# Kernel tuning notes

Measured on AMD Instinct MI355X. Metric: run time of the kernel, lower is better.

The kernel has to match this reference:

```python
import jax, jax.numpy as jnp
import numpy as np

H = 1024        # hidden_size
I = 512         # moe_intermediate_size
E = 16          # n_routed_experts
K = 2           # num_experts_per_tok
N_SHARED = 2    # n_shared_experts
IS = I * N_SHARED  # shared expert intermediate
B, S = 2, 2048


def setup_inputs() -> dict:
    key = jax.random.key(0)
    ks = jax.random.split(key, 9)
    sc = 0.02
    return {
        "hidden_states": jax.random.normal(ks[0], (B, S, H), jnp.float32),
        "router_w":     jax.random.normal(ks[1], (E, H), jnp.float32) * sc,
        "expert_gate":  jax.random.normal(ks[2], (E, H, I), jnp.float32) * sc,
        "expert_up":    jax.random.normal(ks[3], (E, H, I), jnp.float32) * sc,
        "expert_down":  jax.random.normal(ks[4], (E, I, H), jnp.float32) * sc,
        "shared_gate":  jax.random.normal(ks[5], (H, IS), jnp.float32) * sc,
        "shared_up":    jax.random.normal(ks[6], (H, IS), jnp.float32) * sc,
        "shared_down":  jax.random.normal(ks[7], (IS, H), jnp.float32) * sc,
    }


def reference(hidden_states, router_w, expert_gate, expert_up, expert_down,
              shared_gate, shared_up, shared_down):
    orig_shape = hidden_states.shape
    x = hidden_states.reshape(-1, H)            # [T, H]
    T = x.shape[0]

    # --- MoEGate: softmax router scores, top-k, normalized weights ---
    scores = jax.nn.softmax(x @ router_w.T, axis=-1)        # [T, E]
    topk_w, topk_idx = jax.lax.top_k(scores, K)             # [T, K]
    topk_w = topk_w / jnp.sum(topk_w, axis=-1, keepdims=True)  # norm_topk_prob

    # Sparse combine weights as dense [T, E] gate matrix (scatter of top-k).
    gates = jnp.zeros((T, E), x.dtype).at[jnp.arange(T)[:, None], topk_idx].add(topk_w)

    # --- Routed experts: gated SiLU MLP per expert, weighted combine ---
    g = jnp.einsum('th,ehi->tei', x, expert_gate)           # [T, E, I]
    u = jnp.einsum('th,ehi->tei', x, expert_up)             # [T, E, I]
    a = jax.nn.silu(g) * u                                  # [T, E, I]
    y = jnp.einsum('tei,eih,te->th', a, expert_down, gates) # [T, H]

    # --- Shared experts ---
    s = (jax.nn.silu(x @ shared_gate) * (x @ shared_up)) @ shared_down  # [T, H]

    return (y + s).reshape(orig_shape)
```

## Files before the change

### kernel.cpp

```cpp
#include <hip/hip_runtime.h>
#include <hip/hip_bf16.h>
#include <math.h>

#define H_DIM 1024
#define I_DIM 512
#define E_NUM 16
#define T_TOK 4096
#define IS_DIM 1024
#define MAX_GU 1152
#define MAX_DN 1792
#define CSTR 32

typedef unsigned short u16;
typedef __attribute__((ext_vector_type(8))) short short8;
typedef __attribute__((ext_vector_type(4))) float floatx4;

__device__ __forceinline__ float bf2f(u16 u) {
    union { unsigned int u; float f; } c; c.u = ((unsigned int)u) << 16; return c.f;
}
__device__ __forceinline__ u16 f2bf(float f) {
    union { float f; unsigned int u; } c; c.f = f;
    unsigned int r = (c.u + 0x7fffu + ((c.u >> 16) & 1u)) >> 16;
    return (u16)r;
}
__device__ __forceinline__ void gld16(const u16* g, u16* l) {
    __builtin_amdgcn_global_load_lds(
        (const __attribute__((address_space(1))) unsigned int*)g,
        (__attribute__((address_space(3))) unsigned int*)l, 16, 0, 0);
}

__global__ __launch_bounds__(256)
void k_transpose(const float* wg, const float* wu, const float* wd,
                 const float* sg, const float* su, const float* sd,
                 u16* wgt, u16* wut, u16* wdt, u16* sgt, u16* sut, u16* sdt)
{
    int bx = blockIdx.x;
    const float* src; u16* dst; int R, C, local;
    if (bx < 2048)      { src = wg; dst = wgt; R = 1024; C = 512;  local = bx; }
    else if (bx < 4096) { src = wu; dst = wut; R = 1024; C = 512;  local = bx - 2048; }
    else if (bx < 6144) { src = wd; dst = wdt; R = 512;  C = 1024; local = bx - 4096; }
    else if (bx < 6400) { src = sg; dst = sgt; R = 1024; C = 1024; local = bx - 6144; }
    else if (bx < 6656) { src = su; dst = sut; R = 1024; C = 1024; local = bx - 6400; }
    else                { src = sd; dst = sdt; R = 1024; C = 1024; local = bx - 6656; }
    int tpm = (R >> 6) * (C >> 6);
    int mat = local / tpm;
    int tl_ = local - mat * tpm;
    int tcn = C >> 6;
    int tr = tl_ / tcn, tc = tl_ - (tl_ / tcn) * tcn;
    src += (size_t)mat * R * C;
    dst += (size_t)mat * R * C;

    __shared__ u16 tile[64][65];
    int t = threadIdx.x;
    int r0 = t >> 2, c0 = (t & 3) * 16;
    const float* sp = src + (size_t)(tr * 64 + r0) * C + tc * 64 + c0;
    #pragma unroll
    for (int j = 0; j < 16; j += 4) {
        float4 v = *(const float4*)(sp + j);
        tile[r0][c0 + j + 0] = f2bf(v.x);
        tile[r0][c0 + j + 1] = f2bf(v.y);
        tile[r0][c0 + j + 2] = f2bf(v.z);
        tile[r0][c0 + j + 3] = f2bf(v.w);
    }
    __syncthreads();
    int cW = t >> 2, rW = (t & 3) * 16;
    u16 tmp[16];
    #pragma unroll
    for (int j = 0; j < 16; ++j) tmp[j] = tile[rW + j][cW];
    u16* dp = dst + (size_t)(tc * 64 + cW) * R + tr * 64 + rW;
    *(uint4*)(dp)     = *(const uint4*)(tmp);
    *(uint4*)(dp + 8) = *(const uint4*)(tmp + 8);
}

__global__ __launch_bounds__(256)
void k_xconv(const float* x, u16* xb)
{
    int i = blockIdx.x * 256 + threadIdx.x;
    float4 v = ((const float4*)x)[i];
    u16 o[4] = { f2bf(v.x), f2bf(v.y), f2bf(v.z), f2bf(v.w) };
    ((uint2*)xb)[i] = *(const uint2*)o;
}

__global__ __launch_bounds__(256)
void k_router(const float* x, const float* rw, float* topkw, int* elist, int* cnt)
{
    int lane = threadIdx.x & 63;
    int wv = threadIdx.x >> 6;
    int t = blockIdx.x * 4 + wv;
    const float* xr = x + (size_t)t * H_DIM;
    float xv[16];
    #pragma unroll
    for (int j = 0; j < 16; ++j) xv[j] = xr[j * 64 + lane];
    float sc[E_NUM];
    #pragma unroll
    for (int e = 0; e < E_NUM; ++e) sc[e] = 0.f;
    #pragma unroll
    for (int e = 0; e < E_NUM; ++e) {
        const float* rr = rw + e * H_DIM;
        #pragma unroll
        for (int j = 0; j < 16; ++j) sc[e] += xv[j] * rr[j * 64 + lane];
    }
    #pragma unroll
    for (int off = 32; off > 0; off >>= 1) {
        float tmp[E_NUM];
        #pragma unroll
        for (int e = 0; e < E_NUM; ++e) tmp[e] = __shfl_xor(sc[e], off, 64);
        #pragma unroll
        for (int e = 0; e < E_NUM; ++e) sc[e] += tmp[e];
    }
    if (lane == 0) {
        float b1 = -1e30f, b2 = -1e30f; int i1 = 0, i2 = 0;
        #pragma unroll
        for (int e = 0; e < E_NUM; ++e) {
            if (sc[e] > b1) { b2 = b1; i2 = i1; b1 = sc[e]; i1 = e; }
            else if (sc[e] > b2) { b2 = sc[e]; i2 = e; }
        }
        float w1 = 1.f / (1.f + __expf(b2 - b1));
        float w2 = 1.f - w1;
        topkw[t * 2]     = w1;
        topkw[t * 2 + 1] = w2;
        int p1 = atomicAdd(&cnt[i1 * CSTR], 1); elist[i1 * T_TOK + p1] = (t << 1);
        int p2 = atomicAdd(&cnt[i2 * CSTR], 1); elist[i2 * T_TOK + p2] = (t << 1) | 1;
    }
}

__global__ void k_prefix(const int* cnt, int* base,
                         int* gu_desc, int* gu_count, int* dn_desc, int* dn_count)
{
    __shared__ int mts_s[E_NUM], moff_s[E_NUM];
    int lane = threadIdx.x;
    if (lane == 0) {
        int b = 0, mo = 0;
        for (int e = 0; e < E_NUM; ++e) {
            int mts = (cnt[e * CSTR] + 127) >> 7;
            base[e] = b; b += mts << 7;
            mts_s[e] = mts; moff_s[e] = mo; mo += mts;
        }
        *gu_count = 512 + mo * 8;
        *dn_count = 512 + mo * 16;
    }
    __syncthreads();
    for (int i = lane; i < 512; i += 64) {
        int mt = i >> 4, cb = i & 15;
        int d = (1 << 31) | (mt << 8) | cb;
        gu_desc[i] = d;
        dn_desc[i] = d;
    }
    if (lane < E_NUM) {
        int e = lane, mts = mts_s[e], mo = moff_s[e];
        for (int mt = 0; mt < mts; ++mt) {
            #pragma unroll
            for (int cb = 0; cb < 8; ++cb)
                gu_desc[512 + (mo + mt) * 8 + cb] = (e << 16) | (mt << 8) | cb;
            #pragma unroll
            for (int nb = 0; nb < 16; ++nb)
                dn_desc[512 + (mo + mt) * 16 + nb] = (e << 16) | (mt << 8) | nb;
        }
    }
}

__global__ __launch_bounds__(256, 2)
void k_gateup(const u16* xb, const u16* wgt, const u16* wut,
              const u16* sgt, const u16* sut,
              const int* elist, const int* cnt, const int* base,
              const int* gu_desc, const int* gu_count,
              u16* act, u16* sact)
{
    int bi = blockIdx.x;
    if (bi >= *gu_count) return;
    int d = gu_desc[bi];
    int kind = ((unsigned)d) >> 31;
    int e = (d >> 16) & 15, mt = (d >> 8) & 255, cb = d & 255;

    __shared__ u16 lA[128 * 64], lG[64 * 64], lU[64 * 64];
    int tid = threadIdx.x, lane = tid & 63, w = tid >> 6;
    int srow = lane >> 2, scp = lane & 3;

    const u16* gb = kind ? sgt : (wgt + (size_t)e * I_DIM * H_DIM);
    const u16* ub = kind ? sut : (wut + (size_t)e * I_DIM * H_DIM);
    int c = cnt[e * CSTR];

    const u16 *gA[2], *gG, *gU;
    u16 *dA[2], *dG, *dU;
    #pragma unroll
    for (int jj = 0; jj < 2; ++jj) {
        int call = w * 2 + jj;
        int row = call * 16 + srow;
        int gc = scp ^ ((row >> 1) & 3);
        int tok;
        if (kind) tok = mt * 128 + row;
        else {
            int p = mt * 128 + row;
            int pc = p < c ? p : c - 1;
            tok = elist[e * T_TOK + pc] >> 1;
        }
        gA[jj] = xb + (size_t)tok * H_DIM + gc * 8;
        dA[jj] = lA + call * 512;
    }
    {
        int row = w * 16 + srow;
        int gc = scp ^ ((row >> 1) & 3);
        gG = gb + (size_t)(cb * 64 + row) * H_DIM + gc * 8;
        gU = ub + (size_t)(cb * 64 + row) * H_DIM + gc * 8;
        dG = lG + w * 512;
        dU = lU + w * 512;
    }

    int wr = w >> 1, wc = w & 1;
    int quad = lane >> 4, l15 = lane & 15;
    const u16 *fA[4], *fG[2], *fU[2];
    #pragma unroll
    for (int i = 0; i < 4; ++i) {
        int r = wr * 64 + i * 16 + l15;
        fA[i] = lA + r * 32 + (quad ^ ((r >> 1) & 3)) * 8;
    }
    #pragma unroll
    for (int j = 0; j < 2; ++j) {
        int n = wc * 32 + j * 16 + l15;
        fG[j] = lG + n * 32 + (quad ^ ((n >> 1) & 3)) * 8;
        fU[j] = lU + n * 32 + (quad ^ ((n >> 1) & 3)) * 8;
    }

    floatx4 accg[4][2], accu[4][2];
    #pragma unroll
    for (int i = 0; i < 4; ++i)
        #pragma unroll
        for (int j = 0; j < 2; ++j)
            #pragma unroll
            for (int r = 0; r < 4; ++r) { accg[i][j][r] = 0.f; accu[i][j][r] = 0.f; }

    for (int s = 0; s < H_DIM / 64; ++s) {
        #pragma unroll
        for (int q = 0; q < 2; ++q) {
            gld16(gA[0] + q * 32, dA[0] + q * 4096);
            gld16(gA[1] + q * 32, dA[1] + q * 4096);
            gld16(gG + q * 32, dG + q * 2048);
            gld16(gU + q * 32, dU + q * 2048);
        }
        gA[0] += 64; gA[1] += 64; gG += 64; gU += 64;
        __syncthreads();
        #pragma unroll
        for (int q = 0; q < 2; ++q) {
            short8 a[4], g[2], u[2];
            #pragma unroll
            for (int i = 0; i < 4; ++i) a[i] = *(const short8*)(fA[i] + q * 4096);
            #pragma unroll
            for (int j = 0; j < 2; ++j) {
                g[j] = *(const short8*)(fG[j] + q * 2048);
                u[j] = *(const short8*)(fU[j] + q * 2048);
            }
            #pragma unroll
            for (int i = 0; i < 4; ++i)
                #pragma unroll
                for (int j = 0; j < 2; ++j) {
                    accg[i][j] = __builtin_amdgcn_mfma_f32_16x16x32_bf16(a[i], g[j], accg[i][j], 0, 0, 0);
                    accu[i][j] = __builtin_amdgcn_mfma_f32_16x16x32_bf16(a[i], u[j], accu[i][j], 0, 0, 0);
                }
        }
        __syncthreads();
    }

    u16* obase = kind ? (sact + (size_t)(mt * 128) * IS_DIM)
                      : (act + (size_t)(base[e] + mt * 128) * I_DIM);
    int old = kind ? IS_DIM : I_DIM;
    #pragma unroll
    for (int i = 0; i < 4; ++i)
        #pragma unroll
        for (int j = 0; j < 2; ++j)
            #pragma unroll
            for (int r = 0; r < 4; ++r) {
                int row = wr * 64 + i * 16 + quad * 4 + r;
                int col = cb * 64 + wc * 32 + j * 16 + l15;
                float gg = accg[i][j][r], uu = accu[i][j][r];
                float aa = gg / (1.f + __expf(-gg)) * uu;
                obase[(size_t)row * old + col] = f2bf(aa);
            }
}

__global__ __launch_bounds__(256, 2)
void k_down(const u16* act, const u16* sact, const u16* wdt, const u16* sdt,
            const int* elist, const int* cnt, const int* base, const float* topkw,
            const int* dn_desc, const int* dn_count,
            u16* y0, u16* y1, float* out)
{
    int bi = blockIdx.x;
    if (bi >= *dn_count) return;
    int d = dn_desc[bi];
    int kind = ((unsigned)d) >> 31;
    int e = (d >> 16) & 15, mt = (d >> 8) & 255, nb = d & 255;

    __shared__ u16 lA[128 * 64], lB[64 * 64];
    int tid = threadIdx.x, lane = tid & 63, w = tid >> 6;
    int srow = lane >> 2, scp = lane & 3;

    int K = kind ? IS_DIM : I_DIM;
    const u16* ab = kind ? (sact + (size_t)(mt * 128) * IS_DIM)
                         : (act + (size_t)(base[e] + mt * 128) * I_DIM);
    const u16* bb = kind ? (sdt + (size_t)(nb * 64) * IS_DIM)
                         : (wdt + ((size_t)e * H_DIM + nb * 64) * I_DIM);
    int c = cnt[e * CSTR];

    const u16 *gA[2], *gB;
    u16 *dA[2], *dB;
    #pragma unroll
    for (int jj = 0; jj < 2; ++jj) {
        int call = w * 2 + jj;
        int row = call * 16 + srow;
        int gc = scp ^ ((row >> 1) & 3);
        gA[jj] = ab + (size_t)row * K + gc * 8;
        dA[jj] = lA + call * 512;
    }
    {
        int row = w * 16 + srow;
        int gc = scp ^ ((row >> 1) & 3);
        gB = bb + (size_t)row * K + gc * 8;
        dB = lB + w * 512;
    }

    int wr = w >> 1, wc = w & 1;
    int quad = lane >> 4, l15 = lane & 15;
    const u16 *fA[4], *fB[2];
    #pragma unroll
    for (int i = 0; i < 4; ++i) {
        int r = wr * 64 + i * 16 + l15;
        fA[i] = lA + r * 32 + (quad ^ ((r >> 1) & 3)) * 8;
    }
    #pragma unroll
    for (int j = 0; j < 2; ++j) {
        int n = wc * 32 + j * 16 + l15;
        fB[j] = lB + n * 32 + (quad ^ ((n >> 1) & 3)) * 8;
    }

    floatx4 acc[4][2];
    #pragma unroll
    for (int i = 0; i < 4; ++i)
        #pragma unroll
        for (int j = 0; j < 2; ++j)
            #pragma unroll
            for (int r = 0; r < 4; ++r) acc[i][j][r] = 0.f;

    int steps = K >> 6;
    for (int s = 0; s < steps; ++s) {
        #pragma unroll
        for (int q = 0; q < 2; ++q) {
            gld16(gA[0] + q * 32, dA[0] + q * 4096);
            gld16(gA[1] + q * 32, dA[1] + q * 4096);
            gld16(gB + q * 32, dB + q * 2048);
        }
        gA[0] += 64; gA[1] += 64; gB += 64;
        __syncthreads();
        #pragma unroll
        for (int q = 0; q < 2; ++q) {
            short8 a[4], b[2];
            #pragma unroll
            for (int i = 0; i < 4; ++i) a[i] = *(const short8*)(fA[i] + q * 4096);
            #pragma unroll
            for (int j = 0; j < 2; ++j) b[j] = *(const short8*)(fB[j] + q * 2048);
            #pragma unroll
            for (int i = 0; i < 4; ++i)
                #pragma unroll
                for (int j = 0; j < 2; ++j)
                    acc[i][j] = __builtin_amdgcn_mfma_f32_16x16x32_bf16(a[i], b[j], acc[i][j], 0, 0, 0);
        }
        __syncthreads();
    }

    if (kind) {
        #pragma unroll
        for (int i = 0; i < 4; ++i)
            #pragma unroll
            for (int j = 0; j < 2; ++j)
                #pragma unroll
                for (int r = 0; r < 4; ++r) {
                    int row = mt * 128 + wr * 64 + i * 16 + quad * 4 + r;
                    int col = nb * 64 + wc * 32 + j * 16 + l15;
                    out[(size_t)row * H_DIM + col] = acc[i][j][r];
                }
    } else {
        #pragma unroll
        for (int i = 0; i < 4; ++i)
            #pragma unroll
            for (int r = 0; r < 4; ++r) {
                int row = wr * 64 + i * 16 + quad * 4 + r;
                int p = mt * 128 + row;
                if (p < c) {
                    int ent = elist[e * T_TOK + p];
                    int t = ent >> 1, sl = ent & 1;
                    float wt = topkw[t * 2 + sl];
                    u16* yb = sl ? y1 : y0;
                    #pragma unroll
                    for (int j = 0; j < 2; ++j) {
                        int col = nb * 64 + wc * 32 + j * 16 + l15;
                        yb[(size_t)t * H_DIM + col] = f2bf(wt * acc[i][j][r]);
                    }
                }
            }
    }
}

__global__ __launch_bounds__(256)
void k_final(float* out, const u16* y0, const u16* y1)
{
    int i = blockIdx.x * 256 + threadIdx.x;
    float4 o = ((const float4*)out)[i];
    uint2 a = ((const uint2*)y0)[i];
    uint2 b = ((const uint2*)y1)[i];
    const u16* pa = (const u16*)&a;
    const u16* pb = (const u16*)&b;
    o.x += bf2f(pa[0]) + bf2f(pb[0]);
    o.y += bf2f(pa[1]) + bf2f(pb[1]);
    o.z += bf2f(pa[2]) + bf2f(pb[2]);
    o.w += bf2f(pa[3]) + bf2f(pb[3]);
    ((float4*)out)[i] = o;
}

extern "C" void kernel_launch(void* const* d_in, const int* in_sizes, int n_in,
                              void* d_out, int out_size, void* d_ws, size_t ws_size,
                              hipStream_t stream)
{
    const float* x  = (const float*)d_in[0];
    const float* rw = (const float*)d_in[1];
    const float* wg = (const float*)d_in[2];
    const float* wu = (const float*)d_in[3];
    const float* wd = (const float*)d_in[4];
    const float* sg = (const float*)d_in[5];
    const float* su = (const float*)d_in[6];
    const float* sd = (const float*)d_in[7];
    float* out = (float*)d_out;

    char* ws = (char*)d_ws;
    const size_t MB = 1024ull * 1024ull;
    u16* wgt  = (u16*)(ws);
    u16* wut  = (u16*)(ws + 16 * MB);
    u16* wdt  = (u16*)(ws + 32 * MB);
    u16* sgt  = (u16*)(ws + 48 * MB);
    u16* sut  = (u16*)(ws + 50 * MB);
    u16* sdt  = (u16*)(ws + 52 * MB);
    u16* xb   = (u16*)(ws + 54 * MB);
    u16* act  = (u16*)(ws + 62 * MB);
    u16* sact = (u16*)(ws + 72 * MB);
    u16* y0   = (u16*)(ws + 80 * MB);
    u16* y1   = (u16*)(ws + 88 * MB);
    float* topkw  = (float*)(ws + 96 * MB);
    int* elist    = (int*)(ws + 96 * MB + 64 * 1024);
    int* cnt      = (int*)(ws + 97 * MB);
    int* base     = (int*)(ws + 97 * MB + 8192);
    int* gu_count = (int*)(ws + 97 * MB + 8448);
    int* dn_count = (int*)(ws + 97 * MB + 8452);
    int* gu_desc  = (int*)(ws + 97 * MB + 16384);
    int* dn_desc  = (int*)(ws + 97 * MB + 32768);

    hipMemsetAsync(cnt, 0, E_NUM * CSTR * sizeof(int), stream);
    k_transpose<<<6912, 256, 0, stream>>>(wg, wu, wd, sg, su, sd,
                                          wgt, wut, wdt, sgt, sut, sdt);
    k_xconv<<<T_TOK * H_DIM / 4 / 256, 256, 0, stream>>>(x, xb);
    k_router<<<T_TOK / 4, 256, 0, stream>>>(x, rw, topkw, elist, cnt);
    k_prefix<<<1, 64, 0, stream>>>(cnt, base, gu_desc, gu_count, dn_desc, dn_count);
    k_gateup<<<MAX_GU, 256, 0, stream>>>(xb, wgt, wut, sgt, sut,
                                         elist, cnt, base, gu_desc, gu_count,
                                         act, sact);
    k_down<<<MAX_DN, 256, 0, stream>>>(act, sact, wdt, sdt,
                                       elist, cnt, base, topkw,
                                       dn_desc, dn_count, y0, y1, out);
    k_final<<<T_TOK * H_DIM / 4 / 256, 256, 0, stream>>>(out, y0, y1);
}
```

Measured before the change: 291.0 us.

## Fuse prep kernels, derive routed tiles inline, overlap transposes, widen down-proj tiles

Merges the x conversion, router and gate/up/shared weight transposes into one prep kernel, and folds the down-weight transposes into the gate-up launch as extra blocks. It drops the prefix/descriptor kernel by having each block derive its expert tile from the counts inline. The down GEMM tile is widened from 64 to 128 columns to halve block count and improve reuse, and occupancy hints are raised to 3. The intent is fewer launches and overlapping transpose work with GEMM work. The risks are higher register pressure from the larger accumulator and load imbalance from mixing block types in one grid.

```diff
diff --git a/kernel.cpp b/kernel.cpp
--- a/kernel.cpp
+++ b/kernel.cpp
@@ -1,5 +1,4 @@
 #include <hip/hip_runtime.h>
-#include <hip/hip_bf16.h>
 #include <math.h>
 
 #define H_DIM 1024
@@ -7,9 +6,19 @@
 #define E_NUM 16
 #define T_TOK 4096
 #define IS_DIM 1024
-#define MAX_GU 1152
-#define MAX_DN 1792
 #define CSTR 32
+
+#define P_RT   1024
+#define P_WU   (P_RT + 2048)
+#define P_SG   (P_WU + 2048)
+#define P_SU   (P_SG + 256)
+#define P_END  (P_SU + 256)
+
+#define G_TR   2304
+#define G_GEMM 1152
+#define G_END  (G_TR + G_GEMM)
+
+#define D_GRID 896
 
 typedef unsigned short u16;
 typedef __attribute__((ext_vector_type(8))) short short8;
@@ -29,68 +38,80 @@
         (__attribute__((address_space(3))) unsigned int*)l, 16, 0, 0);
 }
 
-__global__ __launch_bounds__(256)
-void k_transpose(const float* wg, const float* wu, const float* wd,
-                 const float* sg, const float* su, const float* sd,
-                 u16* wgt, u16* wut, u16* wdt, u16* sgt, u16* sut, u16* sdt)
-{
-    int bx = blockIdx.x;
-    const float* src; u16* dst; int R, C, local;
-    if (bx < 2048)      { src = wg; dst = wgt; R = 1024; C = 512;  local = bx; }
-    else if (bx < 4096) { src = wu; dst = wut; R = 1024; C = 512;  local = bx - 2048; }
-    else if (bx < 6144) { src = wd; dst = wdt; R = 512;  C = 1024; local = bx - 4096; }
-    else if (bx < 6400) { src = sg; dst = sgt; R = 1024; C = 1024; local = bx - 6144; }
-    else if (bx < 6656) { src = su; dst = sut; R = 1024; C = 1024; local = bx - 6400; }
-    else                { src = sd; dst = sdt; R = 1024; C = 1024; local = bx - 6656; }
+__device__ __forceinline__ void tr64(const float* src, u16* dst, int R, int C,
+                                     int local, u16* tile)
+{
     int tpm = (R >> 6) * (C >> 6);
     int mat = local / tpm;
     int tl_ = local - mat * tpm;
     int tcn = C >> 6;
-    int tr = tl_ / tcn, tc = tl_ - (tl_ / tcn) * tcn;
+    int tr = tl_ / tcn, tc = tl_ - tr * tcn;
     src += (size_t)mat * R * C;
     dst += (size_t)mat * R * C;
-
-    __shared__ u16 tile[64][65];
     int t = threadIdx.x;
-    int r0 = t >> 2, c0 = (t & 3) * 16;
+    int r0 = t >> 2, c0 = (t & 3) << 4;
     const float* sp = src + (size_t)(tr * 64 + r0) * C + tc * 64 + c0;
     #pragma unroll
     for (int j = 0; j < 16; j += 4) {
         float4 v = *(const float4*)(sp + j);
-        tile[r0][c0 + j + 0] = f2bf(v.x);
-        tile[r0][c0 + j + 1] = f2bf(v.y);
-        tile[r0][c0 + j + 2] = f2bf(v.z);
-        tile[r0][c0 + j + 3] = f2bf(v.w);
+        tile[r0 * 65 + c0 + j + 0] = f2bf(v.x);
+        tile[r0 * 65 + c0 + j + 1] = f2bf(v.y);
+        tile[r0 * 65 + c0 + j + 2] = f2bf(v.z);
+        tile[r0 * 65 + c0 + j + 3] = f2bf(v.w);
     }
     __syncthreads();
-    int cW = t >> 2, rW = (t & 3) * 16;
+    int cW = t >> 2, rW = (t & 3) << 4;
     u16 tmp[16];
     #pragma unroll
-    for (int j = 0; j < 16; ++j) tmp[j] = tile[rW + j][cW];
+    for (int j = 0; j < 16; ++j) tmp[j] = tile[(rW + j) * 65 + cW];
     u16* dp = dst + (size_t)(tc * 64 + cW) * R + tr * 64 + rW;
     *(uint4*)(dp)     = *(const uint4*)(tmp);
     *(uint4*)(dp + 8) = *(const uint4*)(tmp + 8);
 }
 
-__global__ __launch_bounds__(256)
-void k_xconv(const float* x, u16* xb)
-{
-    int i = blockIdx.x * 256 + threadIdx.x;
-    float4 v = ((const float4*)x)[i];
-    u16 o[4] = { f2bf(v.x), f2bf(v.y), f2bf(v.z), f2bf(v.w) };
-    ((uint2*)xb)[i] = *(const uint2*)o;
-}
-
-__global__ __launch_bounds__(256)
-void k_router(const float* x, const float* rw, float* topkw, int* elist, int* cnt)
-{
+__device__ __forceinline__ int derive_routed(int gi, const int* cnt,
+                                             int& e, int& mt, int& sub, int& abase)
+{
+    int off = 0, b = 0;
+    #pragma unroll
+    for (int ee = 0; ee < E_NUM; ++ee) {
+        int mts = (cnt[ee * CSTR] + 127) >> 7;
+        int span = mts << 3;
+        if (gi < off + span) {
+            int local = gi - off;
+            e = ee; mt = local >> 3; sub = local & 7; abase = b;
+            return 1;
+        }
+        off += span; b += mts << 7;
+    }
+    return 0;
+}
+
+__global__ __launch_bounds__(256, 4)
+void k_prep(const float* x, const float* rw,
+            const float* wg, const float* wu, const float* sg, const float* su,
+            u16* wgt, u16* wut, u16* sgt, u16* sut,
+            u16* xb, float* topkw, int* elist, int* cnt)
+{
+    __shared__ u16 tile[64 * 65];
+    int bi = blockIdx.x;
+    if (bi >= P_RT) {
+        if (bi < P_WU)      tr64(wg, wgt, 1024, 512,  bi - P_RT, tile);
+        else if (bi < P_SG) tr64(wu, wut, 1024, 512,  bi - P_WU, tile);
+        else if (bi < P_SU) tr64(sg, sgt, 1024, 1024, bi - P_SG, tile);
+        else                tr64(su, sut, 1024, 1024, bi - P_SU, tile);
+        return;
+    }
     int lane = threadIdx.x & 63;
     int wv = threadIdx.x >> 6;
-    int t = blockIdx.x * 4 + wv;
+    int t = bi * 4 + wv;
     const float* xr = x + (size_t)t * H_DIM;
     float xv[16];
     #pragma unroll
     for (int j = 0; j < 16; ++j) xv[j] = xr[j * 64 + lane];
+    u16* xrow = xb + (size_t)t * H_DIM;
+    #pragma unroll
+    for (int j = 0; j < 16; ++j) xrow[j * 64 + lane] = f2bf(xv[j]);
     float sc[E_NUM];
     #pragma unroll
     for (int e = 0; e < E_NUM; ++e) sc[e] = 0.f;
@@ -124,55 +145,31 @@
     }
 }
 
-__global__ void k_prefix(const int* cnt, int* base,
-                         int* gu_desc, int* gu_count, int* dn_desc, int* dn_count)
-{
-    __shared__ int mts_s[E_NUM], moff_s[E_NUM];
-    int lane = threadIdx.x;
-    if (lane == 0) {
-        int b = 0, mo = 0;
-        for (int e = 0; e < E_NUM; ++e) {
-            int mts = (cnt[e * CSTR] + 127) >> 7;
-            base[e] = b; b += mts << 7;
-            mts_s[e] = mts; moff_s[e] = mo; mo += mts;
-        }
-        *gu_count = 512 + mo * 8;
-        *dn_count = 512 + mo * 16;
-    }
-    __syncthreads();
-    for (int i = lane; i < 512; i += 64) {
-        int mt = i >> 4, cb = i & 15;
-        int d = (1 << 31) | (mt << 8) | cb;
-        gu_desc[i] = d;
-        dn_desc[i] = d;
-    }
-    if (lane < E_NUM) {
-        int e = lane, mts = mts_s[e], mo = moff_s[e];
-        for (int mt = 0; mt < mts; ++mt) {
-            #pragma unroll
-            for (int cb = 0; cb < 8; ++cb)
-                gu_desc[512 + (mo + mt) * 8 + cb] = (e << 16) | (mt << 8) | cb;
-            #pragma unroll
-            for (int nb = 0; nb < 16; ++nb)
-                dn_desc[512 + (mo + mt) * 16 + nb] = (e << 16) | (mt << 8) | nb;
-        }
-    }
-}
-
-__global__ __launch_bounds__(256, 2)
+__global__ __launch_bounds__(256, 3)
 void k_gateup(const u16* xb, const u16* wgt, const u16* wut,
               const u16* sgt, const u16* sut,
-              const int* elist, const int* cnt, const int* base,
-              const int* gu_desc, const int* gu_count,
+              const float* wd, const float* sd, u16* wdt, u16* sdt,
+              const int* elist, const int* cnt,
               u16* act, u16* sact)
 {
+    __shared__ u16 smem[128 * 64 + 64 * 64 + 64 * 64];
     int bi = blockIdx.x;
-    if (bi >= *gu_count) return;
-    int d = gu_desc[bi];
-    int kind = ((unsigned)d) >> 31;
-    int e = (d >> 16) & 15, mt = (d >> 8) & 255, cb = d & 255;
-
-    __shared__ u16 lA[128 * 64], lG[64 * 64], lU[64 * 64];
+    if (bi < G_TR) {
+        if (bi < 2048) tr64(wd, wdt, 512, 1024, bi, smem);
+        else           tr64(sd, sdt, 1024, 1024, bi - 2048, smem);
+        return;
+    }
+    int gi = bi - G_TR;
+    int kind, e = 0, mt, cb, abase = 0;
+    if (gi < 512) { kind = 1; mt = gi >> 4; cb = gi & 15; }
+    else {
+        kind = 0;
+        if (!derive_routed(gi - 512, cnt, e, mt, cb, abase)) return;
+    }
+
+    u16* lA = smem;
+    u16* lG = smem + 8192;
+    u16* lU = smem + 12288;
     int tid = threadIdx.x, lane = tid & 63, w = tid >> 6;
     int srow = lane >> 2, scp = lane & 3;
 
@@ -261,7 +258,7 @@
     }
 
     u16* obase = kind ? (sact + (size_t)(mt * 128) * IS_DIM)
-                      : (act + (size_t)(base[e] + mt * 128) * I_DIM);
+                      : (act + (size_t)(abase + mt * 128) * I_DIM);
     int old = kind ? IS_DIM : I_DIM;
     #pragma unroll
     for (int i = 0; i < 4; ++i)
@@ -277,31 +274,34 @@
             }
 }
 
-__global__ __launch_bounds__(256, 2)
+__global__ __launch_bounds__(256, 3)
 void k_down(const u16* act, const u16* sact, const u16* wdt, const u16* sdt,
-            const int* elist, const int* cnt, const int* base, const float* topkw,
-            const int* dn_desc, const int* dn_count,
+            const int* elist, const int* cnt, const float* topkw,
             u16* y0, u16* y1, float* out)
 {
     int bi = blockIdx.x;
-    if (bi >= *dn_count) return;
-    int d = dn_desc[bi];
-    int kind = ((unsigned)d) >> 31;
-    int e = (d >> 16) & 15, mt = (d >> 8) & 255, nb = d & 255;
-
-    __shared__ u16 lA[128 * 64], lB[64 * 64];
+    int kind, e = 0, mt, nb, abase = 0;
+    if (bi < 256) { kind = 1; mt = bi >> 3; nb = bi & 7; }
+    else {
+        kind = 0;
+        if (!derive_routed(bi - 256, cnt, e, mt, nb, abase)) return;
+    }
+
+    __shared__ u16 smem[128 * 64 * 2];
+    u16* lA = smem;
+    u16* lB = smem + 8192;
     int tid = threadIdx.x, lane = tid & 63, w = tid >> 6;
     int srow = lane >> 2, scp = lane & 3;
 
     int K = kind ? IS_DIM : I_DIM;
     const u16* ab = kind ? (sact + (size_t)(mt * 128) * IS_DIM)
-                         : (act + (size_t)(base[e] + mt * 128) * I_DIM);
-    const u16* bb = kind ? (sdt + (size_t)(nb * 64) * IS_DIM)
-                         : (wdt + ((size_t)e * H_DIM + nb * 64) * I_DIM);
+                         : (act + (size_t)(abase + mt * 128) * I_DIM);
+    const u16* bb = kind ? (sdt + (size_t)(nb * 128) * IS_DIM)
+                         : (wdt + ((size_t)e * H_DIM + nb * 128) * I_DIM);
     int c = cnt[e * CSTR];
 
-    const u16 *gA[2], *gB;
-    u16 *dA[2], *dB;
+    const u16 *gA[2], *gB[2];
+    u16 *dA[2], *dB[2];
     #pragma unroll
     for (int jj = 0; jj < 2; ++jj) {
         int call = w * 2 + jj;
@@ -309,33 +309,29 @@
         int gc = scp ^ ((row >> 1) & 3);
         gA[jj] = ab + (size_t)row * K + gc * 8;
         dA[jj] = lA + call * 512;
-    }
-    {
-        int row = w * 16 + srow;
-        int gc = scp ^ ((row >> 1) & 3);
-        gB = bb + (size_t)row * K + gc * 8;
-        dB = lB + w * 512;
+        gB[jj] = bb + (size_t)row * K + gc * 8;
+        dB[jj] = lB + call * 512;
     }
 
     int wr = w >> 1, wc = w & 1;
     int quad = lane >> 4, l15 = lane & 15;
-    const u16 *fA[4], *fB[2];
+    const u16 *fA[4], *fB[4];
     #pragma unroll
     for (int i = 0; i < 4; ++i) {
         int r = wr * 64 + i * 16 + l15;
         fA[i] = lA + r * 32 + (quad ^ ((r >> 1) & 3)) * 8;
     }
     #pragma unroll
-    for (int j = 0; j < 2; ++j) {
-        int n = wc * 32 + j * 16 + l15;
+    for (int j = 0; j < 4; ++j) {
+        int n = wc * 64 + j * 16 + l15;
         fB[j] = lB + n * 32 + (quad ^ ((n >> 1) & 3)) * 8;
     }
 
-    floatx4 acc[4][2];
+    floatx4 acc[4][4];
     #pragma unroll
     for (int i = 0; i < 4; ++i)
         #pragma unroll
-        for (int j = 0; j < 2; ++j)
+        for (int j = 0; j < 4; ++j)
             #pragma unroll
             for (int r = 0; r < 4; ++r) acc[i][j][r] = 0.f;
 
@@ -345,21 +341,22 @@
         for (int q = 0; q < 2; ++q) {
             gld16(gA[0] + q * 32, dA[0] + q * 4096);
             gld16(gA[1] + q * 32, dA[1] + q * 4096);
-            gld16(gB + q * 32, dB + q * 2048);
-        }
-        gA[0] += 64; gA[1] += 64; gB += 64;
+            gld16(gB[0] + q * 32, dB[0] + q * 4096);
+            gld16(gB[1] + q * 32, dB[1] + q * 4096);
+        }
+        gA[0] += 64; gA[1] += 64; gB[0] += 64; gB[1] += 64;
         __syncthreads();
         #pragma unroll
         for (int q = 0; q < 2; ++q) {
-            short8 a[4], b[2];
+            short8 a[4], b[4];
             #pragma unroll
             for (int i = 0; i < 4; ++i) a[i] = *(const short8*)(fA[i] + q * 4096);
             #pragma unroll
-            for (int j = 0; j < 2; ++j) b[j] = *(const short8*)(fB[j] + q * 2048);
+            for (int j = 0; j < 4; ++j) b[j] = *(const short8*)(fB[j] + q * 4096);
             #pragma unroll
             for (int i = 0; i < 4; ++i)
                 #pragma unroll
-                for (int j = 0; j < 2; ++j)
+                for (int j = 0; j < 4; ++j)
                     acc[i][j] = __builtin_amdgcn_mfma_f32_16x16x32_bf16(a[i], b[j], acc[i][j], 0, 0, 0);
         }
         __syncthreads();
@@ -369,11 +366,11 @@
         #pragma unroll
         for (int i = 0; i < 4; ++i)
             #pragma unroll
-            for (int j = 0; j < 2; ++j)
+            for (int j = 0; j < 4; ++j)
                 #pragma unroll
                 for (int r = 0; r < 4; ++r) {
                     int row = mt * 128 + wr * 64 + i * 16 + quad * 4 + r;
-                    int col = nb * 64 + wc * 32 + j * 16 + l15;
+                    int col = nb * 128 + wc * 64 + j * 16 + l15;
                     out[(size_t)row * H_DIM + col] = acc[i][j][r];
                 }
     } else {
@@ -389,8 +386,8 @@
                     float wt = topkw[t * 2 + sl];
                     u16* yb = sl ? y1 : y0;
                     #pragma unroll
-                    for (int j = 0; j < 2; ++j) {
-                        int col = nb * 64 + wc * 32 + j * 16 + l15;
+                    for (int j = 0; j < 4; ++j) {
+                        int col = nb * 128 + wc * 64 + j * 16 + l15;
                         yb[(size_t)t * H_DIM + col] = f2bf(wt * acc[i][j][r]);
                     }
                 }
@@ -444,23 +441,15 @@
     float* topkw  = (float*)(ws + 96 * MB);
     int* elist    = (int*)(ws + 96 * MB + 64 * 1024);
     int* cnt      = (int*)(ws + 97 * MB);
-    int* base     = (int*)(ws + 97 * MB + 8192);
-    int* gu_count = (int*)(ws + 97 * MB + 8448);
-    int* dn_count = (int*)(ws + 97 * MB + 8452);
-    int* gu_desc  = (int*)(ws + 97 * MB + 16384);
-    int* dn_desc  = (int*)(ws + 97 * MB + 32768);
 
     hipMemsetAsync(cnt, 0, E_NUM * CSTR * sizeof(int), stream);
-    k_transpose<<<6912, 256, 0, stream>>>(wg, wu, wd, sg, su, sd,
-                                          wgt, wut, wdt, sgt, sut, sdt);
-    k_xconv<<<T_TOK * H_DIM / 4 / 256, 256, 0, stream>>>(x, xb);
-    k_router<<<T_TOK / 4, 256, 0, stream>>>(x, rw, topkw, elist, cnt);
-    k_prefix<<<1, 64, 0, stream>>>(cnt, base, gu_desc, gu_count, dn_desc, dn_count);
-    k_gateup<<<MAX_GU, 256, 0, stream>>>(xb, wgt, wut, sgt, sut,
-                                         elist, cnt, base, gu_desc, gu_count,
-                                         act, sact);
-    k_down<<<MAX_DN, 256, 0, stream>>>(act, sact, wdt, sdt,
-                                       elist, cnt, base, topkw,
-                                       dn_desc, dn_count, y0, y1, out);
+    k_prep<<<P_END, 256, 0, stream>>>(x, rw, wg, wu, sg, su,
+                                      wgt, wut, sgt, sut,
+                                      xb, topkw, elist, cnt);
+    k_gateup<<<G_END, 256, 0, stream>>>(xb, wgt, wut, sgt, sut,
+                                        wd, sd, wdt, sdt,
+                                        elist, cnt, act, sact);
+    k_down<<<D_GRID, 256, 0, stream>>>(act, sact, wdt, sdt,
+                                       elist, cnt, topkw, y0, y1, out);
     k_final<<<T_TOK * H_DIM / 4 / 256, 256, 0, stream>>>(out, y0, y1);
 }
```

Measured after the change: 273.5 us. -6.0%, faster.
